# Kernel optimization log

Hardware: AMD Instinct MI355X
Metric: run time of the kernel (lower is better)

Reference implementation:

```python
import jax, jax.numpy as jnp
import numpy as np

ALPHA = 0.2  # LeakyReLU negative slope
NEG_INF = -9e15


def setup_inputs() -> dict:
    key = jax.random.key(0)
    k_h, k_adj, k_W, k_a = jax.random.split(key, 4)
    B, N, Din, Dout = 8, 1024, 256, 256
    h = jax.random.normal(k_h, (B, N, Din), dtype=jnp.float32)
    adj = jax.random.randint(k_adj, (B, N, N), 0, 2, dtype=jnp.int32)
    # nn.Linear weight [out, in], xavier-uniform-ish init for a
    W = jax.random.normal(k_W, (Dout, Din), dtype=jnp.float32) * (1.0 / np.sqrt(Din))
    lim = np.float32(1.414 * np.sqrt(6.0 / (2 * Dout + 1)))
    a = jax.random.uniform(k_a, (2 * Dout, 1), dtype=jnp.float32, minval=-lim, maxval=lim)
    return {"h": h, "adj": adj, "W": W, "a": a}


def reference(h, adj, W, a):
    # Wh: [B, N, F]
    Wh = jnp.einsum('bnd,fd->bnf', h, W)
    F_ = Wh.shape[-1]
    # Decompose concat-then-matmul: e_ij = leakyrelu(Wh_i @ a1 + Wh_j @ a2)
    a1 = a[:F_, 0]   # [F]
    a2 = a[F_:, 0]   # [F]
    src = Wh @ a1    # [B, N]  score contribution of row node i
    dst = Wh @ a2    # [B, N]  score contribution of col node j
    e = src[:, :, None] + dst[:, None, :]          # [B, N, N]
    e = jnp.where(e > 0, e, ALPHA * e)             # LeakyReLU
    e = jnp.where(adj > 0, e, NEG_INF)             # mask non-edges
    attention = jax.nn.softmax(e, axis=-1)         # [B, N, N]
    # dropout p=0.0 -> identity in eval/train
    h_prime = jnp.einsum('bij,bjf->bif', attention, Wh)
    return h_prime
```

## Files before the change

kernel.cpp:

```cpp
#include <hip/hip_runtime.h>
#include <hip/hip_bf16.h>
#include <cstdint>

#define ALPHA 0.2f
#define NEG_INF -9000000000000000.0f

typedef __bf16 bf16_t;
typedef __bf16 bf16x8 __attribute__((ext_vector_type(8)));
typedef float f32x16 __attribute__((ext_vector_type(16)));

__global__ __launch_bounds__(256) void k_pre(
    const float* __restrict__ h, const float* __restrict__ W, const float* __restrict__ a,
    const int* __restrict__ adj, bf16_t* __restrict__ WhT,
    float* __restrict__ src, float* __restrict__ dst,
    unsigned long long* __restrict__ mask_ws)
{
  __shared__ __align__(16) char smem[64 * 72 * 2 * sizeof(bf16_t)];
  const int bx = blockIdx.x;
  const int t = threadIdx.x;

  if (bx < 512) {
    bf16_t* WS = (bf16_t*)smem;
    bf16_t* HS = WS + 64 * 72;
    const int b  = bx & 7;
    const int jt = (bx >> 3) & 15;
    const int ft = bx >> 7;
    const int j0 = jt * 64, f0 = ft * 64;
    const int w = t >> 6, lane = t & 63;
    const int mrow = lane & 31, half = lane >> 5;
    const int fsub = (w & 1) * 32, jsub = (w >> 1) * 32;

    const int lr = t >> 2;
    const int lc = (t & 3) * 16;
    const float* wp = W + ((size_t)(f0 + lr)) * 256 + lc;
    const float* hp = h + ((size_t)(b * 1024 + j0 + lr)) * 256 + lc;

    f32x16 acc;
#pragma unroll
    for (int r = 0; r < 16; r++) acc[r] = 0.f;

    for (int s = 0; s < 4; s++) {
      if (s) __syncthreads();
      {
        float4 w0 = *(const float4*)(wp + s * 64);
        float4 w1 = *(const float4*)(wp + s * 64 + 4);
        float4 w2 = *(const float4*)(wp + s * 64 + 8);
        float4 w3 = *(const float4*)(wp + s * 64 + 12);
        bf16x8 va, vb;
        va[0] = (bf16_t)w0.x; va[1] = (bf16_t)w0.y; va[2] = (bf16_t)w0.z; va[3] = (bf16_t)w0.w;
        va[4] = (bf16_t)w1.x; va[5] = (bf16_t)w1.y; va[6] = (bf16_t)w1.z; va[7] = (bf16_t)w1.w;
        vb[0] = (bf16_t)w2.x; vb[1] = (bf16_t)w2.y; vb[2] = (bf16_t)w2.z; vb[3] = (bf16_t)w2.w;
        vb[4] = (bf16_t)w3.x; vb[5] = (bf16_t)w3.y; vb[6] = (bf16_t)w3.z; vb[7] = (bf16_t)w3.w;
        *(bf16x8*)&WS[lr * 72 + lc] = va;
        *(bf16x8*)&WS[lr * 72 + lc + 8] = vb;
        float4 h0 = *(const float4*)(hp + s * 64);
        float4 h1 = *(const float4*)(hp + s * 64 + 4);
        float4 h2 = *(const float4*)(hp + s * 64 + 8);
        float4 h3 = *(const float4*)(hp + s * 64 + 12);
        bf16x8 vc, vd;
        vc[0] = (bf16_t)h0.x; vc[1] = (bf16_t)h0.y; vc[2] = (bf16_t)h0.z; vc[3] = (bf16_t)h0.w;
        vc[4] = (bf16_t)h1.x; vc[5] = (bf16_t)h1.y; vc[6] = (bf16_t)h1.z; vc[7] = (bf16_t)h1.w;
        vd[0] = (bf16_t)h2.x; vd[1] = (bf16_t)h2.y; vd[2] = (bf16_t)h2.z; vd[3] = (bf16_t)h2.w;
        vd[4] = (bf16_t)h3.x; vd[5] = (bf16_t)h3.y; vd[6] = (bf16_t)h3.z; vd[7] = (bf16_t)h3.w;
        *(bf16x8*)&HS[lr * 72 + lc] = vc;
        *(bf16x8*)&HS[lr * 72 + lc + 8] = vd;
      }
      __syncthreads();
#pragma unroll
      for (int ks = 0; ks < 4; ks++) {
        bf16x8 af = *(const bf16x8*)&WS[(fsub + mrow) * 72 + ks * 16 + half * 8];
        bf16x8 bf = *(const bf16x8*)&HS[(jsub + mrow) * 72 + ks * 16 + half * 8];
        acc = __builtin_amdgcn_mfma_f32_32x32x16_bf16(af, bf, acc, 0, 0, 0);
      }
    }

    const int jcol = j0 + jsub + mrow;
#pragma unroll
    for (int r = 0; r < 16; r++) {
      int frow = fsub + (r & 3) + 8 * (r >> 2) + 4 * half;
      WhT[(((size_t)(b * 256 + f0 + frow)) << 10) + jcol] = (bf16_t)acc[r];
    }
  } else {
    float* uS = (float*)smem;
    const int p  = bx - 512;
    const int m0 = p * 16;
    {
      float s1a = 0.f, s1b = 0.f, s2a = 0.f, s2b = 0.f;
#pragma unroll 4
      for (int f = 0; f < 256; f += 2) {
        float w0 = W[f * 256 + t];
        float w1 = W[(f + 1) * 256 + t];
        s1a = fmaf(w0, a[f], s1a);       s1b = fmaf(w1, a[f + 1], s1b);
        s2a = fmaf(w0, a[256 + f], s2a); s2b = fmaf(w1, a[256 + f + 1], s2b);
      }
      uS[t] = s1a + s1b; uS[256 + t] = s2a + s2b;
    }
    __syncthreads();
    {
      const int n = t >> 4, c = t & 15;
      const int m = m0 + n;
      const float* hp = h + (size_t)m * 256 + c * 16;
      float s1 = 0.f, s2 = 0.f;
#pragma unroll
      for (int i = 0; i < 4; i++) {
        float4 v = *(const float4*)(hp + i * 4);
        const float* u1p = &uS[c * 16 + i * 4];
        const float* u2p = &uS[256 + c * 16 + i * 4];
        s1 = fmaf(v.x, u1p[0], s1); s1 = fmaf(v.y, u1p[1], s1);
        s1 = fmaf(v.z, u1p[2], s1); s1 = fmaf(v.w, u1p[3], s1);
        s2 = fmaf(v.x, u2p[0], s2); s2 = fmaf(v.y, u2p[1], s2);
        s2 = fmaf(v.z, u2p[2], s2); s2 = fmaf(v.w, u2p[3], s2);
      }
#pragma unroll
      for (int off = 8; off; off >>= 1) {
        s1 += __shfl_down(s1, off, 16);
        s2 += __shfl_down(s2, off, 16);
      }
      if (c == 0) { src[m] = s1; dst[m] = s2; }
    }
    {
      const int wv = t >> 6, lane = t & 63;
#pragma unroll 4
      for (int r = 0; r < 16; r++) {
        const size_t row = (size_t)(m0 + r);
        const int4 av = *(const int4*)(adj + (row << 10) + 4 * t);
        unsigned long long b0 = __ballot(av.x > 0);
        unsigned long long b1 = __ballot(av.y > 0);
        unsigned long long b2 = __ballot(av.z > 0);
        unsigned long long b3 = __ballot(av.w > 0);
        if (lane == 0) {
          unsigned long long* mp = mask_ws + row * 16 + wv * 4;
          mp[0] = b0; mp[1] = b1; mp[2] = b2; mp[3] = b3;
        }
      }
    }
  }
}

__global__ __launch_bounds__(256) void k_attn(
    const bf16_t* __restrict__ WhT, const float* __restrict__ src, const float* __restrict__ dst,
    const unsigned long long* __restrict__ mask_ws, float* __restrict__ out)
{
  const int b  = blockIdx.x & 7;
  const int fh = (blockIdx.x >> 3) & 1;
  const int i0 = (blockIdx.x >> 4) << 5;
  const int t  = threadIdx.x;
  const int w  = t >> 6;
  const int lane = t & 63;
  const int mrow = lane & 31, half = lane >> 5;

  __shared__ float dstS[1024];
  __shared__ float srcS[32];
  __shared__ unsigned long long maskS[32 * 16];
  __shared__ bf16_t P[2][32 * 264];

  *(float4*)&dstS[t * 4] = *(const float4*)(dst + (b << 10) + t * 4);
  if (t < 32) srcS[t] = src[(b << 10) + i0 + t];
  {
    const size_t mb = ((size_t)(b << 10) + i0) * 16;
    maskS[t]       = mask_ws[mb + t];
    maskS[t + 256] = mask_ws[mb + t + 256];
  }
  __syncthreads();

  f32x16 acc, acc2;
#pragma unroll
  for (int r = 0; r < 16; r++) { acc[r] = 0.f; acc2[r] = 0.f; }

  bf16x8 ones;
#pragma unroll
  for (int k = 0; k < 8; k++) ones[k] = (bf16_t)1.0f;

  const bf16_t* bp = WhT + (((size_t)(b * 256 + fh * 128 + w * 32 + mrow)) << 10);

  for (int c = 0; c < 4; c++) {
    bf16_t* Pc = &P[c & 1][0];
    {
      float dj = dstS[c * 256 + t];
      int mi = c * 4 + (t & 3);
      int sh = t >> 2;
#pragma unroll 8
      for (int i = 0; i < 32; i++) {
        unsigned long long w64 = maskS[i * 16 + mi];
        float v = srcS[i] + dj;
        float vl = fmaxf(v, ALPHA * v);
        float e = ((w64 >> sh) & 1ull) ? vl : NEG_INF;
        Pc[i * 264 + t] = (bf16_t)__expf(e);
      }
    }
    __syncthreads();

    const bf16_t* bpc = bp + c * 256 + half * 8;
    const bf16_t* prow = Pc + mrow * 264 + half * 8;
#pragma unroll
    for (int idx = 0; idx < 16; idx++) {
      bf16x8 afr = *(const bf16x8*)(prow + idx * 16);
      bf16x8 bfr = *(const bf16x8*)(bpc + idx * 16);
      acc  = __builtin_amdgcn_mfma_f32_32x32x16_bf16(afr, bfr, acc, 0, 0, 0);
      acc2 = __builtin_amdgcn_mfma_f32_32x32x16_bf16(afr, ones, acc2, 0, 0, 0);
    }
  }

  const int col = fh * 128 + w * 32 + mrow;
#pragma unroll
  for (int r = 0; r < 16; r++) {
    int row = (r & 3) + 8 * (r >> 2) + 4 * half;
    out[((size_t)(b << 10) + i0 + row) * 256 + col] = acc[r] / acc2[r];
  }
}

extern "C" void kernel_launch(void* const* d_in, const int* in_sizes, int n_in,
                              void* d_out, int out_size, void* d_ws, size_t ws_size,
                              hipStream_t stream) {
  const float* h   = (const float*)d_in[0];
  const int*   adj = (const int*)d_in[1];
  const float* W   = (const float*)d_in[2];
  const float* a   = (const float*)d_in[3];
  float* out = (float*)d_out;

  char* wsb = (char*)d_ws;
  bf16_t* WhT = (bf16_t*)wsb;
  float* srcv = (float*)(wsb + (4u << 20));
  float* dstv = srcv + 8192;
  unsigned long long* mask_ws = (unsigned long long*)(wsb + (4u << 20) + 65536);

  k_pre <<<1024, 256, 0, stream>>>(h, W, a, adj, WhT, srcv, dstv, mask_ws);
  k_attn<<<512,  256, 0, stream>>>(WhT, srcv, dstv, mask_ws, out);
}
```

Baseline: 122.9 us.

## Factor attention exponentials per node and widen attn blocks to all features

Replaces the per-pair LeakyReLU and exp with products of per-node precomputed exponentials, exp(src)*exp(dst) or exp(a*src)*exp(a*dst), picking between them by whether the product exceeds 1. This removes the transcendental from the N×N inner loop. The attention kernel also moves to 512-thread blocks that cover all 256 features, so each probability tile is built once instead of twice, at the cost of half as many blocks. Because there is no max subtraction, large scores could overflow in fp32 or bf16.

```diff
diff --git a/kernel.cpp b/kernel.cpp
--- a/kernel.cpp
+++ b/kernel.cpp
@@ -137,30 +137,32 @@
   }
 }
 
-__global__ __launch_bounds__(256) void k_attn(
+__global__ __launch_bounds__(512) void k_attn(
     const bf16_t* __restrict__ WhT, const float* __restrict__ src, const float* __restrict__ dst,
     const unsigned long long* __restrict__ mask_ws, float* __restrict__ out)
 {
   const int b  = blockIdx.x & 7;
-  const int fh = (blockIdx.x >> 3) & 1;
-  const int i0 = (blockIdx.x >> 4) << 5;
+  const int i0 = (blockIdx.x >> 3) << 5;
   const int t  = threadIdx.x;
   const int w  = t >> 6;
   const int lane = t & 63;
   const int mrow = lane & 31, half = lane >> 5;
 
-  __shared__ float dstS[1024];
-  __shared__ float srcS[32];
+  __shared__ float dstE[1024], dstF[1024];
+  __shared__ float srcE[32], srcF[32];
   __shared__ unsigned long long maskS[32 * 16];
   __shared__ bf16_t P[2][32 * 264];
 
-  *(float4*)&dstS[t * 4] = *(const float4*)(dst + (b << 10) + t * 4);
-  if (t < 32) srcS[t] = src[(b << 10) + i0 + t];
   {
-    const size_t mb = ((size_t)(b << 10) + i0) * 16;
-    maskS[t]       = mask_ws[mb + t];
-    maskS[t + 256] = mask_ws[mb + t + 256];
-  }
+    float2 d2 = *(const float2*)(dst + (b << 10) + t * 2);
+    dstE[t * 2]     = __expf(d2.x);  dstF[t * 2]     = __expf(ALPHA * d2.x);
+    dstE[t * 2 + 1] = __expf(d2.y);  dstF[t * 2 + 1] = __expf(ALPHA * d2.y);
+  }
+  if (t < 32) {
+    float s = src[(b << 10) + i0 + t];
+    srcE[t] = __expf(s);  srcF[t] = __expf(ALPHA * s);
+  }
+  maskS[t] = mask_ws[((size_t)(b << 10) + i0) * 16 + t];
   __syncthreads();
 
   f32x16 acc, acc2;
@@ -171,21 +173,25 @@
 #pragma unroll
   for (int k = 0; k < 8; k++) ones[k] = (bf16_t)1.0f;
 
-  const bf16_t* bp = WhT + (((size_t)(b * 256 + fh * 128 + w * 32 + mrow)) << 10);
+  const bf16_t* bp = WhT + (((size_t)(b * 256 + w * 32 + mrow)) << 10);
+  const int jj = t & 255, ih = t >> 8;
 
   for (int c = 0; c < 4; c++) {
     bf16_t* Pc = &P[c & 1][0];
     {
-      float dj = dstS[c * 256 + t];
-      int mi = c * 4 + (t & 3);
-      int sh = t >> 2;
-#pragma unroll 8
-      for (int i = 0; i < 32; i++) {
+      float Edj = dstE[c * 256 + jj];
+      float Fdj = dstF[c * 256 + jj];
+      int mi = c * 4 + (jj & 3);
+      int sh = jj >> 2;
+#pragma unroll
+      for (int r = 0; r < 16; r++) {
+        int i = ih * 16 + r;
         unsigned long long w64 = maskS[i * 16 + mi];
-        float v = srcS[i] + dj;
-        float vl = fmaxf(v, ALPHA * v);
-        float e = ((w64 >> sh) & 1ull) ? vl : NEG_INF;
-        Pc[i * 264 + t] = (bf16_t)__expf(e);
+        float pp = srcE[i] * Edj;
+        float pn = srcF[i] * Fdj;
+        float p = (pp > 1.0f) ? pp : pn;
+        p = ((w64 >> sh) & 1ull) ? p : 0.0f;
+        Pc[i * 264 + jj] = (bf16_t)p;
       }
     }
     __syncthreads();
@@ -201,7 +207,7 @@
     }
   }
 
-  const int col = fh * 128 + w * 32 + mrow;
+  const int col = w * 32 + mrow;
 #pragma unroll
   for (int r = 0; r < 16; r++) {
     int row = (r & 3) + 8 * (r >> 2) + 4 * half;
@@ -225,5 +231,5 @@
   unsigned long long* mask_ws = (unsigned long long*)(wsb + (4u << 20) + 65536);
 
   k_pre <<<1024, 256, 0, stream>>>(h, W, a, adj, WhT, srcv, dstv, mask_ws);
-  k_attn<<<512,  256, 0, stream>>>(WhT, srcv, dstv, mask_ws, out);
+  k_attn<<<256,  512, 0, stream>>>(WhT, srcv, dstv, mask_ws, out);
 }
```

Result: no change. 121.1 us (-1.4%).
